# Optimization experiments

Hardware: AMD Instinct MI355X
Metric: run time of the kernel (lower is better)

The kernel has to match this reference:

```python
import jax, jax.numpy as jnp
import numpy as np

B, E, K, U = 2048, 96, 8, 1024  # batch, word_emb_size, num_basis, num_units


def setup_inputs() -> dict:
    key = jax.random.key(0)
    k1, k2, k3, k4, k5 = jax.random.split(key, 5)
    inputs = jax.random.normal(k1, (B, E + K), dtype=jnp.float32)
    h_tm1 = jax.random.normal(k2, (B, U), dtype=jnp.float32)
    c_tm1 = jax.random.normal(k3, (B, U), dtype=jnp.float32)
    basis_kernel = jax.random.normal(k4, (E, K, 4 * U), dtype=jnp.float32) * 0.05
    basis_recurrent_kernel = jax.random.normal(k5, (U, K, 4 * U), dtype=jnp.float32) * 0.05
    bias = jnp.zeros((4 * U,), dtype=jnp.float32)
    return {
        "inputs": inputs,
        "h_tm1": h_tm1,
        "c_tm1": c_tm1,
        "basis_kernel": basis_kernel,
        "basis_recurrent_kernel": basis_recurrent_kernel,
        "bias": bias,
    }


def reference(inputs, h_tm1, c_tm1, basis_kernel, basis_recurrent_kernel, bias):
    word_emb_size = basis_kernel.shape[0]
    num_units = basis_recurrent_kernel.shape[0]
    x = inputs[:, :word_emb_size]           # [B, E]
    c_prob = inputs[:, word_emb_size:]      # [B, K]
    # Algebraically identical to composing a per-example kernel
    # (sum_k c_prob[b,k] * W[:,k,:]) and doing a per-example matmul:
    # z[b,z] = sum_e sum_k x[b,e] * c_prob[b,k] * W[e,k,z] (+ recurrent term).
    z = (jnp.einsum('be,ekz,bk->bz', x, basis_kernel, c_prob)
         + jnp.einsum('bu,ukz,bk->bz', h_tm1, basis_recurrent_kernel, c_prob)
         + bias)
    z0, z1, z2, z3 = jnp.split(z, 4, axis=1)  # each [B, U]
    i = jax.nn.sigmoid(z0)
    f = jax.nn.sigmoid(z1)
    c = f * c_tm1 + i * jnp.tanh(z2)
    o = jax.nn.sigmoid(z3)
    h = o * jnp.tanh(c)
    return (h, c)
```

## Files before the change

### kernel.cpp

```cpp
#include <hip/hip_runtime.h>
#include <stdint.h>
#include <stddef.h>

#define B_SZ   2048
#define E_SZ   96
#define K_SZ   8
#define U_SZ   1024
#define EK     (E_SZ * K_SZ)
#define KD     ((E_SZ + U_SZ) * K_SZ)
#define NZ     (4 * U_SZ)

typedef _Float16 f16_t;
typedef _Float16 f16x8 __attribute__((ext_vector_type(8)));
typedef float    f32x4  __attribute__((ext_vector_type(4)));
typedef float    f32x16 __attribute__((ext_vector_type(16)));

typedef __attribute__((address_space(3))) void       lds_void;
typedef const __attribute__((address_space(1))) void gbl_void;

__device__ __forceinline__ void gload16(const void* g, void* l) {
    __builtin_amdgcn_global_load_lds((gbl_void*)g, (lds_void*)l, 16, 0, 0);
}

__global__ __launch_bounds__(256) void build_a_kernel(
    const float* __restrict__ inputs,
    const float* __restrict__ h_tm1,
    f16_t* __restrict__ Ah)
{
    unsigned tid = blockIdx.x * 256u + threadIdx.x;
    unsigned b   = tid / 1120u;
    unsigned i8  = tid - b * 1120u;

    const float* row = inputs + (size_t)b * (E_SZ + K_SZ);
    f32x4 cp0 = *(const f32x4*)(row + E_SZ);
    f32x4 cp1 = *(const f32x4*)(row + E_SZ + 4);
    float cp[8] = {cp0[0], cp0[1], cp0[2], cp0[3], cp1[0], cp1[1], cp1[2], cp1[3]};

    float base = (i8 < (unsigned)E_SZ) ? row[i8]
                                       : h_tm1[(size_t)b * U_SZ + (i8 - E_SZ)];
    f16x8 hi;
    #pragma unroll
    for (int k = 0; k < 8; ++k)
        hi[k] = (f16_t)(base * cp[k]);
    *(f16x8*)(Ah + (size_t)b * KD + (size_t)i8 * 8) = hi;
}

__global__ __launch_bounds__(256) void transpose_w_kernel(
    const float* __restrict__ bk,
    const float* __restrict__ brk,
    f16_t* __restrict__ Wth)
{
    __shared__ float tile[64][65];
    int r0 = blockIdx.x * 64;
    int z0 = blockIdx.y * 64;
    const float* src = (r0 < EK) ? (bk + (size_t)r0 * NZ)
                                 : (brk + (size_t)(r0 - EK) * NZ);
    int t  = threadIdx.x;
    int rl = t >> 4;
    int c4 = (t & 15) * 4;

    #pragma unroll
    for (int i = 0; i < 4; ++i) {
        int r = rl + i * 16;
        f32x4 v = *(const f32x4*)(src + (size_t)r * NZ + z0 + c4);
        tile[r][c4 + 0] = v[0];
        tile[r][c4 + 1] = v[1];
        tile[r][c4 + 2] = v[2];
        tile[r][c4 + 3] = v[3];
    }
    __syncthreads();
    int zl = t >> 3;
    int c8 = (t & 7) * 8;
    #pragma unroll
    for (int i = 0; i < 2; ++i) {
        int z = zl + i * 32;
        f16x8 hi;
        #pragma unroll
        for (int j = 0; j < 8; ++j)
            hi[j] = (f16_t)tile[c8 + j][z];
        *(f16x8*)(Wth + (size_t)(z0 + z) * KD + r0 + c8) = hi;
    }
}

#define BM 256
#define BN 256
#define BK 32
#define KHALF 4480
#define NT 140
#define ABY (BM * BK * 2)
#define WBY (BN * BK * 2)
#define BUFB (ABY + WBY)
#define SMEM_BYTES (4 * BUFB)

__global__ __launch_bounds__(512, 2) void basis_lstm_gemm_kernel(
    const f16_t* __restrict__ Ah, const f16_t* __restrict__ Wth,
    float* __restrict__ zpart)
{
    extern __shared__ __align__(16) char smem[];

    int id   = blockIdx.x;
    int xcd  = id & 7;
    int rest = id >> 3;
    int kh   = rest & 1;
    int bm0  = ((rest >> 1) & 7) * BM;
    int jb   = xcd * 2 + (rest >> 4);
    int kbase = kh * KHALF;
    float* zp = zpart + (size_t)kh * B_SZ * NZ;

    int t    = threadIdx.x;
    int lane = t & 63;
    int w    = t >> 6;
    int wm   = w & 1;
    int wn   = w >> 1;
    int l31  = lane & 31;
    int lh   = lane >> 5;

    f32x16 acc[4][2];
    #pragma unroll
    for (int mi = 0; mi < 4; ++mi)
        #pragma unroll
        for (int ni = 0; ni < 2; ++ni)
            #pragma unroll
            for (int e = 0; e < 16; ++e)
                acc[mi][ni][e] = 0.f;

    auto stage = [&](int kt) {
        char* buf = smem + (kt & 3) * BUFB;
        int   ko  = kbase + kt * BK;
        #pragma unroll
        for (int i = 0; i < 2; ++i) {
            int q = i * 512 + t;
            int row = q >> 2, cc = q & 3;
            size_t off = (size_t)(bm0 + row) * KD + ko + ((cc ^ ((row ^ (row >> 2)) & 3)) << 3);
            gload16(Ah + off, buf + q * 16);
        }
        #pragma unroll
        for (int i = 0; i < 2; ++i) {
            int q = i * 512 + t;
            int c = q >> 2, cc = q & 3;
            int z = ((c >> 6) << 10) + jb * 64 + (c & 63);
            size_t off = (size_t)z * KD + ko + ((cc ^ ((c ^ (c >> 2)) & 3)) << 3);
            gload16(Wth + off, buf + ABY + q * 16);
        }
    };

    auto cslice = [&](const char* buf, int ks) {
        f16x8 af[4], wf[2];
        #pragma unroll
        for (int mi = 0; mi < 4; ++mi) {
            int r  = wm * 128 + mi * 32 + l31;
            int sc = (ks * 2 + lh) ^ ((r ^ (r >> 2)) & 3);
            af[mi] = *(const f16x8*)(buf + r * 64 + sc * 16);
        }
        #pragma unroll
        for (int ni = 0; ni < 2; ++ni) {
            int c  = wn * 64 + ni * 32 + l31;
            int sc = (ks * 2 + lh) ^ ((c ^ (c >> 2)) & 3);
            wf[ni] = *(const f16x8*)(buf + ABY + c * 64 + sc * 16);
        }
        __builtin_amdgcn_s_setprio(1);
        #pragma unroll
        for (int mi = 0; mi < 4; ++mi)
            #pragma unroll
            for (int ni = 0; ni < 2; ++ni)
                acc[mi][ni] = __builtin_amdgcn_mfma_f32_32x32x16_f16(af[mi], wf[ni], acc[mi][ni], 0, 0, 0);
        __builtin_amdgcn_s_setprio(0);
    };

    stage(0); stage(1); stage(2);
    asm volatile("s_waitcnt vmcnt(8)" ::: "memory");
    __builtin_amdgcn_s_barrier();

    #pragma unroll 1
    for (int kt = 0; kt < NT; ++kt) {
        if (kt + 3 < NT) stage(kt + 3);
        const char* buf = smem + (kt & 3) * BUFB;
        cslice(buf, 0);
        cslice(buf, 1);
        if (kt <= NT - 4) {
            asm volatile("s_waitcnt vmcnt(8)" ::: "memory");
        } else if (kt == NT - 3) {
            asm volatile("s_waitcnt vmcnt(4)" ::: "memory");
        } else if (kt == NT - 2) {
            asm volatile("s_waitcnt vmcnt(0)" ::: "memory");
        }
        if (kt < NT - 1) __builtin_amdgcn_s_barrier();
    }

    #pragma unroll
    for (int ni = 0; ni < 2; ++ni) {
        int c    = wn * 64 + ni * 32 + l31;
        int zcol = ((c >> 6) << 10) + jb * 64 + (c & 63);
        #pragma unroll
        for (int mi = 0; mi < 4; ++mi) {
            #pragma unroll
            for (int r = 0; r < 16; ++r) {
                int row = wm * 128 + mi * 32 + (r & 3) + 8 * (r >> 2) + 4 * lh;
                zp[(size_t)(bm0 + row) * NZ + zcol] = acc[mi][ni][r];
            }
        }
    }
}

__global__ __launch_bounds__(256) void lstm_reduce_kernel(
    const float* __restrict__ zpart, const float* __restrict__ bias,
    const float* __restrict__ c_tm1, float* __restrict__ out)
{
    int b  = blockIdx.x;
    int j4 = threadIdx.x * 4;
    const float* zp0 = zpart + (size_t)b * NZ;
    const float* zp1 = zpart + (size_t)B_SZ * NZ + (size_t)b * NZ;

    f32x4 zg[4];
    #pragma unroll
    for (int g = 0; g < 4; ++g) {
        f32x4 a = *(const f32x4*)(zp0 + g * U_SZ + j4);
        f32x4 c = *(const f32x4*)(zp1 + g * U_SZ + j4);
        f32x4 bb = *(const f32x4*)(bias + g * U_SZ + j4);
        zg[g] = a + c + bb;
    }
    f32x4 cprev = *(const f32x4*)(c_tm1 + (size_t)b * U_SZ + j4);
    f32x4 ho, co;
    #pragma unroll
    for (int e = 0; e < 4; ++e) {
        float ig = 1.f / (1.f + __expf(-zg[0][e]));
        float fg = 1.f / (1.f + __expf(-zg[1][e]));
        float og = 1.f / (1.f + __expf(-zg[3][e]));
        float cn = fg * cprev[e] + ig * tanhf(zg[2][e]);
        co[e] = cn;
        ho[e] = og * tanhf(cn);
    }
    *(f32x4*)(out + (size_t)b * U_SZ + j4) = ho;
    *(f32x4*)(out + (size_t)B_SZ * U_SZ + (size_t)b * U_SZ + j4) = co;
}

extern "C" void kernel_launch(void* const* d_in, const int* in_sizes, int n_in,
                              void* d_out, int out_size, void* d_ws, size_t ws_size,
                              hipStream_t stream) {
    const float* inputs = (const float*)d_in[0];
    const float* h_tm1  = (const float*)d_in[1];
    const float* c_tm1  = (const float*)d_in[2];
    const float* bk     = (const float*)d_in[3];
    const float* brk    = (const float*)d_in[4];
    const float* bias   = (const float*)d_in[5];

    char*  ws    = (char*)d_ws;
    f16_t* Ah    = (f16_t*)(ws);
    f16_t* Wth   = (f16_t*)(ws + 36700160u);
    float* zpart = (float*)(ws + 36700160u + 73400320u);

    hipFuncSetAttribute((const void*)basis_lstm_gemm_kernel,
                        hipFuncAttributeMaxDynamicSharedMemorySize, SMEM_BYTES);

    hipLaunchKernelGGL(build_a_kernel, dim3(8960), dim3(256), 0, stream,
                       inputs, h_tm1, Ah);
    hipLaunchKernelGGL(transpose_w_kernel, dim3(140, 64), dim3(256), 0, stream,
                       bk, brk, Wth);
    hipLaunchKernelGGL(basis_lstm_gemm_kernel, dim3(256), dim3(512), SMEM_BYTES, stream,
                       Ah, Wth, zpart);
    hipLaunchKernelGGL(lstm_reduce_kernel, dim3(B_SZ), dim3(256), 0, stream,
                       zpart, bias, c_tm1, (float*)d_out);
}
```

Before: 418.1 us.

## Restructure GEMM main loop into double-buffered 64-wide K tiles with sub-stage interleaving

The GEMM K tile grows from 32 to 64 and the ring of four buffers becomes two 64KB buffers, each split into four sub-tiles (two halves each for A and W). Each loop iteration now issues global-to-LDS loads for the next tile one quarter at a time, interleaved with LDS fragment reads and MFMA blocks, with a barrier per sub-step and sched_barriers to pin the order. The warp-to-tile mapping also changes from a 2x4 to a 4-major layout, which alters which waves share rows versus columns. The aim is finer-grained overlap of memory and compute with fewer outer iterations. The cost is less prefetch depth (one tile ahead instead of three) and four barriers per tile instead of one.

```diff
diff --git a/kernel.cpp b/kernel.cpp
--- a/kernel.cpp
+++ b/kernel.cpp
@@ -84,13 +84,12 @@
 
 #define BM 256
 #define BN 256
-#define BK 32
+#define BK 64
 #define KHALF 4480
-#define NT 140
-#define ABY (BM * BK * 2)
-#define WBY (BN * BK * 2)
-#define BUFB (ABY + WBY)
-#define SMEM_BYTES (4 * BUFB)
+#define NT 70
+#define SUBT 16384
+#define BUFB 65536
+#define SMEM_BYTES 131072
 
 __global__ __launch_bounds__(512, 2) void basis_lstm_gemm_kernel(
     const f16_t* __restrict__ Ah, const f16_t* __restrict__ Wth,
@@ -110,8 +109,8 @@
     int t    = threadIdx.x;
     int lane = t & 63;
     int w    = t >> 6;
-    int wm   = w & 1;
-    int wn   = w >> 1;
+    int wm   = w >> 2;
+    int wn   = w & 3;
     int l31  = lane & 31;
     int lh   = lane >> 5;
 
@@ -124,67 +123,74 @@
             for (int e = 0; e < 16; ++e)
                 acc[mi][ni][e] = 0.f;
 
-    auto stage = [&](int kt) {
-        char* buf = smem + (kt & 3) * BUFB;
-        int   ko  = kbase + kt * BK;
-        #pragma unroll
-        for (int i = 0; i < 2; ++i) {
-            int q = i * 512 + t;
-            int row = q >> 2, cc = q & 3;
-            size_t off = (size_t)(bm0 + row) * KD + ko + ((cc ^ ((row ^ (row >> 2)) & 3)) << 3);
-            gload16(Ah + off, buf + q * 16);
-        }
-        #pragma unroll
-        for (int i = 0; i < 2; ++i) {
-            int q = i * 512 + t;
-            int c = q >> 2, cc = q & 3;
-            int z = ((c >> 6) << 10) + jb * 64 + (c & 63);
-            size_t off = (size_t)z * KD + ko + ((cc ^ ((c ^ (c >> 2)) & 3)) << 3);
-            gload16(Wth + off, buf + ABY + q * 16);
+    auto stage_half = [&](int kt, int s) {
+        char* buf = smem + (kt & 1) * BUFB;
+        int   h   = s >> 1;
+        int   ko  = kbase + kt * BK + h * 32;
+        if (!(s & 1)) {
+            char* dst = buf + h * SUBT;
+            #pragma unroll
+            for (int i = 0; i < 2; ++i) {
+                int q = i * 512 + t;
+                int row = q >> 2, cl = q & 3;
+                size_t off = (size_t)(bm0 + row) * KD + ko + ((cl ^ ((row ^ (row >> 2)) & 3)) << 3);
+                gload16(Ah + off, dst + q * 16);
+            }
+        } else {
+            char* dst = buf + 2 * SUBT + h * SUBT;
+            #pragma unroll
+            for (int i = 0; i < 2; ++i) {
+                int q = i * 512 + t;
+                int c = q >> 2, cl = q & 3;
+                int z = ((c >> 6) << 10) + jb * 64 + (c & 63);
+                size_t off = (size_t)z * KD + ko + ((cl ^ ((c ^ (c >> 2)) & 3)) << 3);
+                gload16(Wth + off, dst + q * 16);
+            }
         }
     };
 
-    auto cslice = [&](const char* buf, int ks) {
-        f16x8 af[4], wf[2];
-        #pragma unroll
-        for (int mi = 0; mi < 4; ++mi) {
-            int r  = wm * 128 + mi * 32 + l31;
-            int sc = (ks * 2 + lh) ^ ((r ^ (r >> 2)) & 3);
-            af[mi] = *(const f16x8*)(buf + r * 64 + sc * 16);
-        }
-        #pragma unroll
-        for (int ni = 0; ni < 2; ++ni) {
-            int c  = wn * 64 + ni * 32 + l31;
-            int sc = (ks * 2 + lh) ^ ((c ^ (c >> 2)) & 3);
-            wf[ni] = *(const f16x8*)(buf + ABY + c * 64 + sc * 16);
-        }
-        __builtin_amdgcn_s_setprio(1);
-        #pragma unroll
-        for (int mi = 0; mi < 4; ++mi)
-            #pragma unroll
-            for (int ni = 0; ni < 2; ++ni)
-                acc[mi][ni] = __builtin_amdgcn_mfma_f32_32x32x16_f16(af[mi], wf[ni], acc[mi][ni], 0, 0, 0);
-        __builtin_amdgcn_s_setprio(0);
-    };
-
-    stage(0); stage(1); stage(2);
-    asm volatile("s_waitcnt vmcnt(8)" ::: "memory");
+    stage_half(0, 0); stage_half(0, 1); stage_half(0, 2); stage_half(0, 3);
+    asm volatile("s_waitcnt vmcnt(4)" ::: "memory");
     __builtin_amdgcn_s_barrier();
+    __builtin_amdgcn_sched_barrier(0);
 
     #pragma unroll 1
     for (int kt = 0; kt < NT; ++kt) {
-        if (kt + 3 < NT) stage(kt + 3);
-        const char* buf = smem + (kt & 3) * BUFB;
-        cslice(buf, 0);
-        cslice(buf, 1);
-        if (kt <= NT - 4) {
-            asm volatile("s_waitcnt vmcnt(8)" ::: "memory");
-        } else if (kt == NT - 3) {
-            asm volatile("s_waitcnt vmcnt(4)" ::: "memory");
-        } else if (kt == NT - 2) {
-            asm volatile("s_waitcnt vmcnt(0)" ::: "memory");
+        const char* buf = smem + (kt & 1) * BUFB;
+        #pragma unroll
+        for (int s = 0; s < 4; ++s) {
+            const char* abase = buf + (s >> 1) * SUBT;
+            const char* bbase = buf + 2 * SUBT + (s >> 1) * SUBT;
+            int cchunk = (s & 1) * 2 + lh;
+            f16x8 af[4], wf[2];
+            #pragma unroll
+            for (int mi = 0; mi < 4; ++mi) {
+                int r = wm * 128 + mi * 32 + l31;
+                af[mi] = *(const f16x8*)(abase + r * 64 + ((cchunk ^ ((r ^ (r >> 2)) & 3)) << 4));
+            }
+            #pragma unroll
+            for (int ni = 0; ni < 2; ++ni) {
+                int c = wn * 64 + ni * 32 + l31;
+                wf[ni] = *(const f16x8*)(bbase + c * 64 + ((cchunk ^ ((c ^ (c >> 2)) & 3)) << 4));
+            }
+            if (kt + 1 < NT) stage_half(kt + 1, s);
+            if (s == 1) {
+                if (kt + 1 < NT) asm volatile("s_waitcnt vmcnt(4)" ::: "memory");
+                else             asm volatile("s_waitcnt vmcnt(0)" ::: "memory");
+            } else if (s == 3) {
+                if (kt + 1 < NT) asm volatile("s_waitcnt vmcnt(4)" ::: "memory");
+            }
+            __builtin_amdgcn_sched_barrier(0);
+            __builtin_amdgcn_s_barrier();
+            __builtin_amdgcn_sched_barrier(0);
+            __builtin_amdgcn_s_setprio(1);
+            #pragma unroll
+            for (int mi = 0; mi < 4; ++mi)
+                #pragma unroll
+                for (int ni = 0; ni < 2; ++ni)
+                    acc[mi][ni] = __builtin_amdgcn_mfma_f32_32x32x16_f16(af[mi], wf[ni], acc[mi][ni], 0, 0, 0);
+            __builtin_amdgcn_s_setprio(0);
         }
-        if (kt < NT - 1) __builtin_amdgcn_s_barrier();
     }
 
     #pragma unroll
```

Measured after the change: 409.9 us. -2.0%, faster.
